# Kernel tuning notes

Hardware: AMD Instinct MI355X
Metric: run time of the kernel (lower is better)

The kernel has to match this reference:

```python
import jax, jax.numpy as jnp
import numpy as np

B, N, C, H = 4, 1024, 512, 8
HD = C // H
SCALE = HD ** -0.5
LN_EPS = 1e-5


def setup_inputs() -> dict:
    key = jax.random.key(0)
    ks = jax.random.split(key, 4)
    return {
        "x": jax.random.normal(ks[0], (B, N, C), dtype=jnp.float32),
        "Wqkv": jax.random.normal(ks[1], (C, 3 * C), dtype=jnp.float32) * (C ** -0.5),
        "bqkv": jnp.zeros((3 * C,), dtype=jnp.float32),
        "order_weights": jnp.ones((3,), dtype=jnp.float32),
        "Wproj": jax.random.normal(ks[2], (C, C), dtype=jnp.float32) * (C ** -0.5),
        "bproj": jnp.zeros((C,), dtype=jnp.float32),
        "gamma": jnp.ones((C,), dtype=jnp.float32),
        "beta": jnp.zeros((C,), dtype=jnp.float32),
    }


def reference(x, Wqkv, bqkv, order_weights, Wproj, bproj, gamma, beta):
    b, n, c = x.shape
    qkv = (x @ Wqkv + bqkv).reshape(b, n, 3, H, HD)
    qkv = jnp.transpose(qkv, (2, 0, 3, 1, 4))  # [3, B, H, N, HD]
    q, k, v = qkv[0], qkv[1], qkv[2]

    base = jnp.einsum('bhnd,bhmd->bhnm', q, k) * SCALE  # [B, H, N, N]

    ow = jax.nn.softmax(order_weights)
    # torch loop: term_0 = base, term_i = base**(i+1)
    attn = ow[0] * base
    cur = base
    for i in range(1, order_weights.shape[0]):
        cur = cur * base
        attn = attn + ow[i] * cur

    attn_final = jax.nn.softmax(attn, axis=-1)

    out = jnp.einsum('bhnm,bhmd->bhnd', attn_final, v)
    out = jnp.transpose(out, (0, 2, 1, 3)).reshape(b, n, c)
    out = out @ Wproj + bproj

    y = x + out
    mu = jnp.mean(y, axis=-1, keepdims=True)
    var = jnp.var(y, axis=-1, keepdims=True)
    y = (y - mu) / jnp.sqrt(var + LN_EPS) * gamma + beta
    return y, attn_final
```

## Files before the change

### kernel.cpp

```cpp
#include <hip/hip_runtime.h>
#include <math.h>

#define B_ 4
#define N_ 1024
#define C_ 512
#define H_ 8
#define HD_ 64
#define SCALE_ 0.125f
#define LN_EPS_ 1e-5f

typedef _Float16 f16x8 __attribute__((ext_vector_type(8)));
typedef float f32x4 __attribute__((ext_vector_type(4)));

__device__ __forceinline__ void cvt_split(const float4& A, const float4& Bv,
                                          f16x8& hi, f16x8& lo) {
    float v[8] = {A.x, A.y, A.z, A.w, Bv.x, Bv.y, Bv.z, Bv.w};
#pragma unroll
    for (int i = 0; i < 8; ++i) {
        _Float16 h = (_Float16)v[i];
        hi[i] = h;
        lo[i] = (_Float16)(v[i] - (float)h);
    }
}

__global__ __launch_bounds__(256) void wsplit_qkv(const float* __restrict__ W,
                                                  _Float16* __restrict__ wt_hi,
                                                  _Float16* __restrict__ wt_lo) {
    __shared__ float tile[64][65];
    const int tid = threadIdx.x;
    const int n0 = blockIdx.x * 64;
    const int k0 = blockIdx.y * 64;
#pragma unroll
    for (int i = 0; i < 16; ++i) {
        int e = tid + i * 256;
        int kk = e >> 6, nn = e & 63;
        tile[kk][nn] = W[(size_t)(k0 + kk) * (3 * C_) + n0 + nn];
    }
    __syncthreads();
#pragma unroll
    for (int i = 0; i < 16; ++i) {
        int e = tid + i * 256;
        int n = e >> 6, k = e & 63;
        float v = tile[k][n];
        _Float16 h = (_Float16)v;
        wt_hi[(size_t)(n0 + n) * C_ + k0 + k] = h;
        wt_lo[(size_t)(n0 + n) * C_ + k0 + k] = (_Float16)(v - (float)h);
    }
}

__global__ __launch_bounds__(256) void wsplit_proj(const float* __restrict__ W,
                                                   _Float16* __restrict__ wp_hi,
                                                   _Float16* __restrict__ wp_lo) {
    __shared__ float tile[64][65];
    const int tid = threadIdx.x;
    const int n0 = blockIdx.x * 64;
    const int k0 = blockIdx.y * 64;
#pragma unroll
    for (int i = 0; i < 16; ++i) {
        int e = tid + i * 256;
        int kk = e >> 6, nn = e & 63;
        tile[kk][nn] = W[(size_t)(k0 + kk) * C_ + n0 + nn];
    }
    __syncthreads();
#pragma unroll
    for (int i = 0; i < 16; ++i) {
        int e = tid + i * 256;
        int n = e >> 6, k = e & 63;
        float v = tile[k][n];
        _Float16 h = (_Float16)v;
        wp_hi[(size_t)(n0 + n) * C_ + k0 + k] = h;
        wp_lo[(size_t)(n0 + n) * C_ + k0 + k] = (_Float16)(v - (float)h);
    }
}

__global__ __launch_bounds__(256) void vsplit_v(const float* __restrict__ qkv,
                                                _Float16* __restrict__ vt_hi,
                                                _Float16* __restrict__ vt_lo) {
    __shared__ float tile[64][65];
    const int tid = threadIdx.x;
    const int m0 = blockIdx.x * 64;
    const int bh = blockIdx.y;
    const int b = bh >> 3, h = bh & 7;
    const size_t RS = 3 * C_;
#pragma unroll
    for (int i = 0; i < 16; ++i) {
        int e = tid + i * 256;
        int mm = e >> 6, d = e & 63;
        tile[mm][d] = qkv[(size_t)(b * N_ + m0 + mm) * RS + 2 * C_ + h * HD_ + d];
    }
    __syncthreads();
#pragma unroll
    for (int i = 0; i < 16; ++i) {
        int e = tid + i * 256;
        int d = e >> 6, mm = e & 63;
        float v = tile[mm][d];
        _Float16 hh = (_Float16)v;
        size_t idx = ((size_t)bh * HD_ + d) * N_ + m0 + mm;
        vt_hi[idx] = hh;
        vt_lo[idx] = (_Float16)(v - (float)hh);
    }
}

__global__ __launch_bounds__(256) void qkv_gemm_mfma(const float* __restrict__ x,
                                                     const _Float16* __restrict__ wt_hi,
                                                     const _Float16* __restrict__ wt_lo,
                                                     const float* __restrict__ bqkv,
                                                     float* __restrict__ qkv) {
    const int tid = threadIdx.x;
    const int lane = tid & 63;
    const int w = tid >> 6;
    const int r16 = lane & 15;
    const int g = lane >> 4;
    const int row0 = blockIdx.x * 32;
    const int col0 = blockIdx.y * 256 + w * 64;

    f32x4 acc[2][4] = {};

    const float* xr0 = x + (size_t)(row0 + r16) * C_;
    const float* xr1 = x + (size_t)(row0 + 16 + r16) * C_;

    for (int kt = 0; kt < 16; ++kt) {
        const int k0 = kt * 32 + 8 * g;
        f16x8 aHi0, aLo0, aHi1, aLo1;
        {
            float4 a0 = *(const float4*)&xr0[k0];
            float4 a1 = *(const float4*)&xr0[k0 + 4];
            cvt_split(a0, a1, aHi0, aLo0);
            float4 b0 = *(const float4*)&xr1[k0];
            float4 b1 = *(const float4*)&xr1[k0 + 4];
            cvt_split(b0, b1, aHi1, aLo1);
        }
#pragma unroll
        for (int ct = 0; ct < 4; ++ct) {
            const int c = col0 + ct * 16 + r16;
            f16x8 bHi = *(const f16x8*)&wt_hi[(size_t)c * C_ + k0];
            f16x8 bLo = *(const f16x8*)&wt_lo[(size_t)c * C_ + k0];
            acc[0][ct] = __builtin_amdgcn_mfma_f32_16x16x32_f16(aHi0, bHi, acc[0][ct], 0, 0, 0);
            acc[0][ct] = __builtin_amdgcn_mfma_f32_16x16x32_f16(aHi0, bLo, acc[0][ct], 0, 0, 0);
            acc[0][ct] = __builtin_amdgcn_mfma_f32_16x16x32_f16(aLo0, bHi, acc[0][ct], 0, 0, 0);
            acc[1][ct] = __builtin_amdgcn_mfma_f32_16x16x32_f16(aHi1, bHi, acc[1][ct], 0, 0, 0);
            acc[1][ct] = __builtin_amdgcn_mfma_f32_16x16x32_f16(aHi1, bLo, acc[1][ct], 0, 0, 0);
            acc[1][ct] = __builtin_amdgcn_mfma_f32_16x16x32_f16(aLo1, bHi, acc[1][ct], 0, 0, 0);
        }
    }

#pragma unroll
    for (int rt = 0; rt < 2; ++rt)
#pragma unroll
        for (int ct = 0; ct < 4; ++ct) {
            const int c = col0 + ct * 16 + r16;
            const float bias = bqkv[c];
#pragma unroll
            for (int j = 0; j < 4; ++j) {
                const int r = row0 + rt * 16 + 4 * g + j;
                qkv[(size_t)r * (3 * C_) + c] = acc[rt][ct][j] + bias;
            }
        }
}

__global__ __launch_bounds__(256) void attn_scores(const float* __restrict__ qkv,
                                                   const float* __restrict__ ow_in,
                                                   float* __restrict__ attn) {
    __shared__ float smax[4][16];
    __shared__ float ssum[4][16];

    const int tid = threadIdx.x;
    const int lane = tid & 63;
    const int w = tid >> 6;
    const int r16 = lane & 15;
    const int g = lane >> 4;
    const int n0 = blockIdx.x * 16;
    const int bh = blockIdx.y;
    const int b = bh >> 3, h = bh & 7;
    const size_t RS = 3 * C_;

    float w0 = ow_in[0], w1 = ow_in[1], w2 = ow_in[2];
    float wm = fmaxf(w0, fmaxf(w1, w2));
    float e0 = __expf(w0 - wm), e1 = __expf(w1 - wm), e2 = __expf(w2 - wm);
    float einv = 1.0f / (e0 + e1 + e2);
    float ow0 = e0 * einv, ow1 = e1 * einv, ow2 = e2 * einv;

    const float* qrow = qkv + (size_t)(b * N_ + n0 + r16) * RS + h * HD_;
    f16x8 aHi0, aLo0, aHi1, aLo1;
    {
        float4 qa = ((const float4*)qrow)[2 * g + 0];
        float4 qb = ((const float4*)qrow)[2 * g + 1];
        float4 qc = ((const float4*)qrow)[8 + 2 * g];
        float4 qd = ((const float4*)qrow)[9 + 2 * g];
        cvt_split(qa, qb, aHi0, aLo0);
        cvt_split(qc, qd, aHi1, aLo1);
    }

    float p[16][4];

    const float* kbase = qkv + (size_t)(b * N_) * RS + C_ + h * HD_;
#pragma unroll
    for (int t = 0; t < 16; ++t) {
        const int ct = w * 16 + t;
        const float* krow = kbase + (size_t)(ct * 16 + r16) * RS;
        float4 ka = ((const float4*)krow)[2 * g + 0];
        float4 kb = ((const float4*)krow)[2 * g + 1];
        float4 kc = ((const float4*)krow)[8 + 2 * g];
        float4 kd = ((const float4*)krow)[9 + 2 * g];
        f16x8 bHi0, bLo0, bHi1, bLo1;
        cvt_split(ka, kb, bHi0, bLo0);
        cvt_split(kc, kd, bHi1, bLo1);

        f32x4 acc = {0.f, 0.f, 0.f, 0.f};
        acc = __builtin_amdgcn_mfma_f32_16x16x32_f16(aHi0, bHi0, acc, 0, 0, 0);
        acc = __builtin_amdgcn_mfma_f32_16x16x32_f16(aHi0, bLo0, acc, 0, 0, 0);
        acc = __builtin_amdgcn_mfma_f32_16x16x32_f16(aLo0, bHi0, acc, 0, 0, 0);
        acc = __builtin_amdgcn_mfma_f32_16x16x32_f16(aHi1, bHi1, acc, 0, 0, 0);
        acc = __builtin_amdgcn_mfma_f32_16x16x32_f16(aHi1, bLo1, acc, 0, 0, 0);
        acc = __builtin_amdgcn_mfma_f32_16x16x32_f16(aLo1, bHi1, acc, 0, 0, 0);

#pragma unroll
        for (int j = 0; j < 4; ++j) {
            float s = acc[j] * SCALE_;
            p[t][j] = s * (ow0 + s * (ow1 + s * ow2));
        }
    }

    float rmax[4] = {-1e30f, -1e30f, -1e30f, -1e30f};
#pragma unroll
    for (int t = 0; t < 16; ++t)
#pragma unroll
        for (int j = 0; j < 4; ++j) rmax[j] = fmaxf(rmax[j], p[t][j]);
#pragma unroll
    for (int j = 0; j < 4; ++j)
#pragma unroll
        for (int m = 1; m < 16; m <<= 1)
            rmax[j] = fmaxf(rmax[j], __shfl_xor(rmax[j], m, 64));
    if (r16 == 0) {
#pragma unroll
        for (int j = 0; j < 4; ++j) smax[w][g * 4 + j] = rmax[j];
    }
    __syncthreads();
    float gm[4];
#pragma unroll
    for (int j = 0; j < 4; ++j) {
        int rr = g * 4 + j;
        gm[j] = fmaxf(fmaxf(smax[0][rr], smax[1][rr]),
                      fmaxf(smax[2][rr], smax[3][rr]));
    }

    float rsum[4] = {0.f, 0.f, 0.f, 0.f};
#pragma unroll
    for (int t = 0; t < 16; ++t)
#pragma unroll
        for (int j = 0; j < 4; ++j) {
            float e = __expf(p[t][j] - gm[j]);
            p[t][j] = e;
            rsum[j] += e;
        }
#pragma unroll
    for (int j = 0; j < 4; ++j)
#pragma unroll
        for (int m = 1; m < 16; m <<= 1)
            rsum[j] += __shfl_xor(rsum[j], m, 64);
    if (r16 == 0) {
#pragma unroll
        for (int j = 0; j < 4; ++j) ssum[w][g * 4 + j] = rsum[j];
    }
    __syncthreads();
    float inv[4];
#pragma unroll
    for (int j = 0; j < 4; ++j) {
        int rr = g * 4 + j;
        inv[j] = 1.0f / (ssum[0][rr] + ssum[1][rr] + ssum[2][rr] + ssum[3][rr]);
    }

    float* abase = attn + ((size_t)bh * N_ + n0 + 4 * g) * N_ + w * 256 + r16;
#pragma unroll
    for (int j = 0; j < 4; ++j) {
        float* arow = abase + (size_t)j * N_;
        float sc = inv[j];
#pragma unroll
        for (int t = 0; t < 16; ++t)
            arow[t * 16] = p[t][j] * sc;
    }
}

__global__ __launch_bounds__(256) void pv_mfma(const float* __restrict__ attn,
                                               const _Float16* __restrict__ vt_hi,
                                               const _Float16* __restrict__ vt_lo,
                                               float* __restrict__ ctx) {
    __shared__ float red[4][16][68];

    const int tid = threadIdx.x;
    const int lane = tid & 63;
    const int w = tid >> 6;
    const int r16 = lane & 15;
    const int g = lane >> 4;
    const int n0 = blockIdx.x * 16;
    const int bh = blockIdx.y;
    const int b = bh >> 3, h = bh & 7;

    const float* prow = attn + ((size_t)bh * N_ + n0 + r16) * N_ + w * 256 + 8 * g;
    const _Float16* vh = vt_hi + (size_t)bh * HD_ * N_ + w * 256 + 8 * g;
    const _Float16* vl = vt_lo + (size_t)bh * HD_ * N_ + w * 256 + 8 * g;

    f32x4 acc[4] = {};

#pragma unroll
    for (int grp = 0; grp < 2; ++grp) {
        float4 p0[4], p1[4];
#pragma unroll
        for (int u = 0; u < 4; ++u) {
            const int k0 = (grp * 4 + u) * 32;
            p0[u] = *(const float4*)&prow[k0];
            p1[u] = *(const float4*)&prow[k0 + 4];
        }
#pragma unroll
        for (int u = 0; u < 4; ++u) {
            const int k0 = (grp * 4 + u) * 32;
            f16x8 aHi, aLo;
            cvt_split(p0[u], p1[u], aHi, aLo);
#pragma unroll
            for (int ct = 0; ct < 4; ++ct) {
                const int d = ct * 16 + r16;
                f16x8 bHi = *(const f16x8*)&vh[(size_t)d * N_ + k0];
                f16x8 bLo = *(const f16x8*)&vl[(size_t)d * N_ + k0];
                acc[ct] = __builtin_amdgcn_mfma_f32_16x16x32_f16(aHi, bHi, acc[ct], 0, 0, 0);
                acc[ct] = __builtin_amdgcn_mfma_f32_16x16x32_f16(aHi, bLo, acc[ct], 0, 0, 0);
                acc[ct] = __builtin_amdgcn_mfma_f32_16x16x32_f16(aLo, bHi, acc[ct], 0, 0, 0);
            }
        }
    }

#pragma unroll
    for (int ct = 0; ct < 4; ++ct)
#pragma unroll
        for (int j = 0; j < 4; ++j)
            red[w][4 * g + j][ct * 16 + r16] = acc[ct][j];
    __syncthreads();

    const int e = tid * 4;
    const int row = e >> 6;
    const int d = e & 63;
    float4 s0 = *(const float4*)&red[0][row][d];
    float4 s1 = *(const float4*)&red[1][row][d];
    float4 s2 = *(const float4*)&red[2][row][d];
    float4 s3 = *(const float4*)&red[3][row][d];
    float4 o;
    o.x = s0.x + s1.x + s2.x + s3.x;
    o.y = s0.y + s1.y + s2.y + s3.y;
    o.z = s0.z + s1.z + s2.z + s3.z;
    o.w = s0.w + s1.w + s2.w + s3.w;
    *(float4*)&ctx[(size_t)(b * N_ + n0 + row) * C_ + h * HD_ + d] = o;
}

__global__ __launch_bounds__(256) void proj_mfma(const float* __restrict__ ctx,
                                                 const float* __restrict__ x,
                                                 const _Float16* __restrict__ wp_hi,
                                                 const _Float16* __restrict__ wp_lo,
                                                 const float* __restrict__ bproj,
                                                 float* __restrict__ y) {
    const int tid = threadIdx.x;
    const int lane = tid & 63;
    const int w = tid >> 6;
    const int r16 = lane & 15;
    const int g = lane >> 4;
    const int row0 = blockIdx.x * 32;
    const int colw = blockIdx.y * 128 + w * 32;

    f32x4 acc[2][2] = {};

    const float* ar0 = ctx + (size_t)(row0 + r16) * C_;
    const float* ar1 = ctx + (size_t)(row0 + 16 + r16) * C_;

    for (int kt = 0; kt < 16; kt += 2) {
        float4 a0[2], a1[2], b0[2], b1[2];
#pragma unroll
        for (int u = 0; u < 2; ++u) {
            const int k0 = (kt + u) * 32 + 8 * g;
            a0[u] = *(const float4*)&ar0[k0];
            a1[u] = *(const float4*)&ar0[k0 + 4];
            b0[u] = *(const float4*)&ar1[k0];
            b1[u] = *(const float4*)&ar1[k0 + 4];
        }
#pragma unroll
        for (int u = 0; u < 2; ++u) {
            const int k0 = (kt + u) * 32 + 8 * g;
            f16x8 aHi0, aLo0, aHi1, aLo1;
            cvt_split(a0[u], a1[u], aHi0, aLo0);
            cvt_split(b0[u], b1[u], aHi1, aLo1);
#pragma unroll
            for (int ct = 0; ct < 2; ++ct) {
                const int c = colw + ct * 16 + r16;
                f16x8 bHi = *(const f16x8*)&wp_hi[(size_t)c * C_ + k0];
                f16x8 bLo = *(const f16x8*)&wp_lo[(size_t)c * C_ + k0];
                acc[0][ct] = __builtin_amdgcn_mfma_f32_16x16x32_f16(aHi0, bHi, acc[0][ct], 0, 0, 0);
                acc[0][ct] = __builtin_amdgcn_mfma_f32_16x16x32_f16(aHi0, bLo, acc[0][ct], 0, 0, 0);
                acc[0][ct] = __builtin_amdgcn_mfma_f32_16x16x32_f16(aLo0, bHi, acc[0][ct], 0, 0, 0);
                acc[1][ct] = __builtin_amdgcn_mfma_f32_16x16x32_f16(aHi1, bHi, acc[1][ct], 0, 0, 0);
                acc[1][ct] = __builtin_amdgcn_mfma_f32_16x16x32_f16(aHi1, bLo, acc[1][ct], 0, 0, 0);
                acc[1][ct] = __builtin_amdgcn_mfma_f32_16x16x32_f16(aLo1, bHi, acc[1][ct], 0, 0, 0);
            }
        }
    }

#pragma unroll
    for (int rt = 0; rt < 2; ++rt)
#pragma unroll
        for (int ct = 0; ct < 2; ++ct) {
            const int c = colw + ct * 16 + r16;
            const float bias = bproj[c];
#pragma unroll
            for (int j = 0; j < 4; ++j) {
                const int r = row0 + rt * 16 + 4 * g + j;
                y[(size_t)r * C_ + c] = acc[rt][ct][j] + bias + x[(size_t)r * C_ + c];
            }
        }
}

__global__ __launch_bounds__(256) void ln_kernel(float* __restrict__ y,
                                                 const float* __restrict__ gamma,
                                                 const float* __restrict__ beta) {
    __shared__ float wsum[4], wsq[4];
    const int row = blockIdx.x;
    const int tid = threadIdx.x;
    const int lane = tid & 63;
    const int w = tid >> 6;

    float2 v = ((const float2*)(y + (size_t)row * C_))[tid];
    float s = v.x + v.y;
    float sq = v.x * v.x + v.y * v.y;
#pragma unroll
    for (int m = 1; m < 64; m <<= 1) {
        s += __shfl_xor(s, m, 64);
        sq += __shfl_xor(sq, m, 64);
    }
    if (lane == 0) { wsum[w] = s; wsq[w] = sq; }
    __syncthreads();
    float ts = wsum[0] + wsum[1] + wsum[2] + wsum[3];
    float tq = wsq[0] + wsq[1] + wsq[2] + wsq[3];
    float mu = ts * (1.0f / C_);
    float var = tq * (1.0f / C_) - mu * mu;
    float rstd = rsqrtf(var + LN_EPS_);

    float2 g = ((const float2*)gamma)[tid];
    float2 be = ((const float2*)beta)[tid];
    float2 o;
    o.x = (v.x - mu) * rstd * g.x + be.x;
    o.y = (v.y - mu) * rstd * g.y + be.y;
    ((float2*)(y + (size_t)row * C_))[tid] = o;
}

extern "C" void kernel_launch(void* const* d_in, const int* in_sizes, int n_in,
                              void* d_out, int out_size, void* d_ws, size_t ws_size,
                              hipStream_t stream) {
    const float* x     = (const float*)d_in[0];
    const float* Wqkv  = (const float*)d_in[1];
    const float* bqkv  = (const float*)d_in[2];
    const float* ow    = (const float*)d_in[3];
    const float* Wproj = (const float*)d_in[4];
    const float* bproj = (const float*)d_in[5];
    const float* gamma = (const float*)d_in[6];
    const float* beta  = (const float*)d_in[7];

    float* out  = (float*)d_out;
    float* y    = out;
    float* attn = out + (size_t)B_ * N_ * C_;
    float* qkv  = (float*)d_ws;
    float* ctx  = qkv + (size_t)B_ * N_ * 3 * C_;

    _Float16* wt_hi = (_Float16*)attn;
    _Float16* wt_lo = wt_hi + (size_t)(3 * C_) * C_;
    _Float16* vt_hi = (_Float16*)y;
    _Float16* vt_lo = vt_hi + (size_t)B_ * H_ * HD_ * N_;
    _Float16* wp_hi = (_Float16*)(ctx + (size_t)B_ * N_ * C_);
    _Float16* wp_lo = wp_hi + (size_t)C_ * C_;

    dim3 g0(3 * C_ / 64, C_ / 64);
    wsplit_qkv<<<g0, 256, 0, stream>>>(Wqkv, wt_hi, wt_lo);

    dim3 gp(C_ / 64, C_ / 64);
    wsplit_proj<<<gp, 256, 0, stream>>>(Wproj, wp_hi, wp_lo);

    dim3 g1(B_ * N_ / 32, 3 * C_ / 256);
    qkv_gemm_mfma<<<g1, 256, 0, stream>>>(x, wt_hi, wt_lo, bqkv, qkv);

    dim3 gv(N_ / 64, B_ * H_);
    vsplit_v<<<gv, 256, 0, stream>>>(qkv, vt_hi, vt_lo);

    dim3 g2(N_ / 16, B_ * H_);
    attn_scores<<<g2, 256, 0, stream>>>(qkv, ow, attn);

    dim3 g3(N_ / 16, B_ * H_);
    pv_mfma<<<g3, 256, 0, stream>>>(attn, vt_hi, vt_lo, ctx);

    dim3 g4(B_ * N_ / 32, C_ / 128);
    proj_mfma<<<g4, 256, 0, stream>>>(ctx, x, wp_hi, wp_lo, bproj, y);

    ln_kernel<<<B_ * N_, 256, 0, stream>>>(y, gamma, beta);
}
```

Baseline: 399.4 us.

## Fuse PV matmul into attention scores kernel via LDS transpose of probabilities

Merges the separate PV kernel into the attention-score kernel. Normalized probabilities held in registers are staged through a per-wave LDS buffer, re-laid-out into MFMA A-operand format, split to hi/lo fp16 and multiplied with V, and the cross-wave reduction reuses the same buffer. This removes one launch and the full re-read of the attention matrix from global memory, at the cost of a larger LDS footprint (about 36KB per block) that can lower occupancy, plus extra LDS traffic.

```diff
diff --git a/kernel.cpp b/kernel.cpp
--- a/kernel.cpp
+++ b/kernel.cpp
@@ -160,9 +160,13 @@
 
 __global__ __launch_bounds__(256) void attn_scores(const float* __restrict__ qkv,
                                                    const float* __restrict__ ow_in,
-                                                   float* __restrict__ attn) {
+                                                   const _Float16* __restrict__ vt_hi,
+                                                   const _Float16* __restrict__ vt_lo,
+                                                   float* __restrict__ attn,
+                                                   float* __restrict__ ctx) {
     __shared__ float smax[4][16];
     __shared__ float ssum[4][16];
+    __shared__ float Pw[4][16][140];
 
     const int tid = threadIdx.x;
     const int lane = tid & 63;
@@ -270,57 +274,48 @@
         inv[j] = 1.0f / (ssum[0][rr] + ssum[1][rr] + ssum[2][rr] + ssum[3][rr]);
     }
 
+#pragma unroll
+    for (int t = 0; t < 16; ++t)
+#pragma unroll
+        for (int j = 0; j < 4; ++j)
+            p[t][j] *= inv[j];
+
     float* abase = attn + ((size_t)bh * N_ + n0 + 4 * g) * N_ + w * 256 + r16;
 #pragma unroll
     for (int j = 0; j < 4; ++j) {
         float* arow = abase + (size_t)j * N_;
-        float sc = inv[j];
 #pragma unroll
         for (int t = 0; t < 16; ++t)
-            arow[t * 16] = p[t][j] * sc;
-    }
-}
-
-__global__ __launch_bounds__(256) void pv_mfma(const float* __restrict__ attn,
-                                               const _Float16* __restrict__ vt_hi,
-                                               const _Float16* __restrict__ vt_lo,
-                                               float* __restrict__ ctx) {
-    __shared__ float red[4][16][68];
-
-    const int tid = threadIdx.x;
-    const int lane = tid & 63;
-    const int w = tid >> 6;
-    const int r16 = lane & 15;
-    const int g = lane >> 4;
-    const int n0 = blockIdx.x * 16;
-    const int bh = blockIdx.y;
-    const int b = bh >> 3, h = bh & 7;
-
-    const float* prow = attn + ((size_t)bh * N_ + n0 + r16) * N_ + w * 256 + 8 * g;
+            arow[t * 16] = p[t][j];
+    }
+
     const _Float16* vh = vt_hi + (size_t)bh * HD_ * N_ + w * 256 + 8 * g;
     const _Float16* vl = vt_lo + (size_t)bh * HD_ * N_ + w * 256 + 8 * g;
+    float* pw = &Pw[w][0][0];
 
     f32x4 acc[4] = {};
 
 #pragma unroll
-    for (int grp = 0; grp < 2; ++grp) {
-        float4 p0[4], p1[4];
-#pragma unroll
-        for (int u = 0; u < 4; ++u) {
-            const int k0 = (grp * 4 + u) * 32;
-            p0[u] = *(const float4*)&prow[k0];
-            p1[u] = *(const float4*)&prow[k0 + 4];
-        }
-#pragma unroll
-        for (int u = 0; u < 4; ++u) {
-            const int k0 = (grp * 4 + u) * 32;
+    for (int half = 0; half < 2; ++half) {
+#pragma unroll
+        for (int t8 = 0; t8 < 8; ++t8) {
+            const int t = half * 8 + t8;
+#pragma unroll
+            for (int j = 0; j < 4; ++j)
+                pw[(4 * g + j) * 140 + t8 * 16 + r16] = p[t][j];
+        }
+#pragma unroll
+        for (int kk = 0; kk < 4; ++kk) {
+            float4 q0 = *(const float4*)&pw[r16 * 140 + kk * 32 + 8 * g];
+            float4 q1 = *(const float4*)&pw[r16 * 140 + kk * 32 + 8 * g + 4];
             f16x8 aHi, aLo;
-            cvt_split(p0[u], p1[u], aHi, aLo);
+            cvt_split(q0, q1, aHi, aLo);
+            const int kb = half * 128 + kk * 32;
 #pragma unroll
             for (int ct = 0; ct < 4; ++ct) {
                 const int d = ct * 16 + r16;
-                f16x8 bHi = *(const f16x8*)&vh[(size_t)d * N_ + k0];
-                f16x8 bLo = *(const f16x8*)&vl[(size_t)d * N_ + k0];
+                f16x8 bHi = *(const f16x8*)&vh[(size_t)d * N_ + kb];
+                f16x8 bLo = *(const f16x8*)&vl[(size_t)d * N_ + kb];
                 acc[ct] = __builtin_amdgcn_mfma_f32_16x16x32_f16(aHi, bHi, acc[ct], 0, 0, 0);
                 acc[ct] = __builtin_amdgcn_mfma_f32_16x16x32_f16(aHi, bLo, acc[ct], 0, 0, 0);
                 acc[ct] = __builtin_amdgcn_mfma_f32_16x16x32_f16(aLo, bHi, acc[ct], 0, 0, 0);
@@ -332,16 +327,20 @@
     for (int ct = 0; ct < 4; ++ct)
 #pragma unroll
         for (int j = 0; j < 4; ++j)
-            red[w][4 * g + j][ct * 16 + r16] = acc[ct][j];
+            pw[(4 * g + j) * 68 + ct * 16 + r16] = acc[ct][j];
     __syncthreads();
 
     const int e = tid * 4;
     const int row = e >> 6;
     const int d = e & 63;
-    float4 s0 = *(const float4*)&red[0][row][d];
-    float4 s1 = *(const float4*)&red[1][row][d];
-    float4 s2 = *(const float4*)&red[2][row][d];
-    float4 s3 = *(const float4*)&red[3][row][d];
+    const float* r0 = &Pw[0][0][0];
+    const float* r1 = &Pw[1][0][0];
+    const float* r2 = &Pw[2][0][0];
+    const float* r3 = &Pw[3][0][0];
+    float4 s0 = *(const float4*)&r0[row * 68 + d];
+    float4 s1 = *(const float4*)&r1[row * 68 + d];
+    float4 s2 = *(const float4*)&r2[row * 68 + d];
+    float4 s3 = *(const float4*)&r3[row * 68 + d];
     float4 o;
     o.x = s0.x + s1.x + s2.x + s3.x;
     o.y = s0.y + s1.y + s2.y + s3.y;
@@ -485,10 +484,7 @@
     vsplit_v<<<gv, 256, 0, stream>>>(qkv, vt_hi, vt_lo);
 
     dim3 g2(N_ / 16, B_ * H_);
-    attn_scores<<<g2, 256, 0, stream>>>(qkv, ow, attn);
-
-    dim3 g3(N_ / 16, B_ * H_);
-    pv_mfma<<<g3, 256, 0, stream>>>(attn, vt_hi, vt_lo, ctx);
+    attn_scores<<<g2, 256, 0, stream>>>(qkv, ow, vt_hi, vt_lo, attn, ctx);
 
     dim3 g4(B_ * N_ / 32, C_ / 128);
     proj_mfma<<<g4, 256, 0, stream>>>(ctx, x, wp_hi, wp_lo, bproj, y);
```

Measured after the change: 382.9 us. 4.1% less time.
